# Kernel tuning notes

Measured on AMD Instinct MI355X. Metric: run time of the kernel, lower is better.

## Reference

```python
import jax, jax.numpy as jnp
import numpy as np

N, E = 50000, 400000
FN, FE = 128, 128          # in/out node and edge feature dims
W = 256                     # fnns_width
EPS = 1e-5


def _layer_norm(x, g, b):
    m = x.mean(-1, keepdims=True)
    var = x.var(-1, keepdims=True)
    return (x - m) / jnp.sqrt(var + EPS) * g + b


def _fnn(x, params):
    # FNN applies ReLU after EVERY linear, including the last one.
    for w, b in params:
        x = jax.nn.relu(x @ w + b)
    return x


def setup_inputs() -> dict:
    key = jax.random.key(0)
    ks = jax.random.split(key, 32)
    s = 0.05
    d = {
        'v': jax.random.normal(ks[0], (N, FN), jnp.float32),
        'e': jax.random.normal(ks[1], (E, FE), jnp.float32),
        'edge_index': jax.random.randint(ks[2], (2, E), 0, N, jnp.int32),
        # edge branch: LayerNorm over concat width FE + 2*FN = 384
        'edge_ln_g': jnp.ones((FE + 2 * FN,), jnp.float32),
        'edge_ln_b': jnp.zeros((FE + 2 * FN,), jnp.float32),
        'ew0': jax.random.normal(ks[3], (FE + 2 * FN, W), jnp.float32) * s,
        'eb0': jnp.zeros((W,), jnp.float32),
        'ew1': jax.random.normal(ks[4], (W, W), jnp.float32) * s,
        'eb1': jnp.zeros((W,), jnp.float32),
        'ew2': jax.random.normal(ks[5], (W, FE), jnp.float32) * s,
        'eb2': jnp.zeros((FE,), jnp.float32),
        'edge_linear': jax.random.normal(ks[6], (FE, FE), jnp.float32) * s,
        # node branch: LayerNorm over concat width FE + FN = 256
        'node_ln_g': jnp.ones((FE + FN,), jnp.float32),
        'node_ln_b': jnp.zeros((FE + FN,), jnp.float32),
        'nw0': jax.random.normal(ks[7], (FE + FN, W), jnp.float32) * s,
        'nb0': jnp.zeros((W,), jnp.float32),
        'nw1': jax.random.normal(ks[8], (W, W), jnp.float32) * s,
        'nb1': jnp.zeros((W,), jnp.float32),
        'nw2': jax.random.normal(ks[9], (W, FN), jnp.float32) * s,
        'nb2': jnp.zeros((FN,), jnp.float32),
        'node_linear': jax.random.normal(ks[10], (FN, FN), jnp.float32) * s,
    }
    return d


def reference(v, e, edge_index, edge_ln_g, edge_ln_b, ew0, eb0, ew1, eb1,
              ew2, eb2, edge_linear, node_ln_g, node_ln_b, nw0, nb0, nw1,
              nb1, nw2, nb2, node_linear):
    row, col = edge_index[0], edge_index[1]
    n = v.shape[0]
    # edge update: residual linear + FNN(LayerNorm(concat))
    edge_in = jnp.concatenate([e, v[row], v[col]], axis=-1)  # [E, 384]
    e_new = e @ edge_linear + _fnn(
        _layer_norm(edge_in, edge_ln_g, edge_ln_b),
        [(ew0, eb0), (ew1, eb1), (ew2, eb2)])
    # mean scatter-aggregate over destination nodes (col)
    counts = jax.ops.segment_sum(jnp.ones((e.shape[0],), e.dtype), col,
                                 num_segments=n)
    e_aggr = jax.ops.segment_sum(e_new, col, num_segments=n)
    e_aggr = e_aggr / jnp.clip(counts, 1.0)[:, None]
    # node update
    node_in = jnp.concatenate([e_aggr, v], axis=-1)  # [N, 256]
    v_new = v @ node_linear + _fnn(
        _layer_norm(node_in, node_ln_g, node_ln_b),
        [(nw0, nb0), (nw1, nb1), (nw2, nb2)])
    return (v_new, e_new)
```

## Files before the change

kernel.cpp:

```cpp
#include <hip/hip_runtime.h>

typedef _Float16 f16_t;
typedef f16_t f16x4 __attribute__((ext_vector_type(4)));
typedef f16_t f16x8 __attribute__((ext_vector_type(8)));
typedef float f32x4 __attribute__((ext_vector_type(4)));

#define MFMA16(a, b, c) __builtin_amdgcn_mfma_f32_16x16x32_f16((a), (b), (c), 0, 0, 0)

__device__ __forceinline__ float bfr(float x) { return (float)(__bf16)x; }

__global__ void pack_weights_kernel(
    const float* __restrict__ ew0, const float* __restrict__ ew1,
    const float* __restrict__ ew2, const float* __restrict__ eL,
    const float* __restrict__ nw0, const float* __restrict__ nw1,
    const float* __restrict__ nw2, const float* __restrict__ nL,
    f16_t* __restrict__ dst)
{
    int tid = blockIdx.x * 256 + threadIdx.x;
    int fid = tid >> 6, lane = tid & 63;
    const float* src; int Ncols, foff, doff;
    if (fid < 192)      { src = ew0; Ncols = 256; foff = 0;   doff = 0;      }
    else if (fid < 320) { src = ew1; Ncols = 256; foff = 192; doff = 98304;  }
    else if (fid < 384) { src = ew2; Ncols = 128; foff = 320; doff = 163840; }
    else if (fid < 416) { src = eL;  Ncols = 128; foff = 384; doff = 196608; }
    else if (fid < 544) { src = nw0; Ncols = 256; foff = 416; doff = 212992; }
    else if (fid < 672) { src = nw1; Ncols = 256; foff = 544; doff = 278528; }
    else if (fid < 736) { src = nw2; Ncols = 128; foff = 672; doff = 344064; }
    else                { src = nL;  Ncols = 128; foff = 736; doff = 376832; }
    int f = fid - foff;
    int NT = Ncols >> 4;
    int kstep = f / NT, ntile = f - kstep * NT;
    int col = ntile * 16 + (lane & 15);
    int kbase = kstep * 32 + ((lane >> 4) << 3);
    f16x8 out;
    #pragma unroll
    for (int j = 0; j < 8; ++j)
        out[j] = (f16_t)bfr(src[(size_t)(kbase + j) * Ncols + col]);
    *reinterpret_cast<f16x8*>(dst + (size_t)doff + ((size_t)f * 64 + lane) * 8) = out;
}

__global__ void pack_params_kernel(
    const float* __restrict__ elng, const float* __restrict__ elnb,
    const float* __restrict__ eb0,  const float* __restrict__ eb1,
    const float* __restrict__ eb2,  const float* __restrict__ nlng,
    const float* __restrict__ nlnb, const float* __restrict__ nb0,
    const float* __restrict__ nb1,  const float* __restrict__ nb2,
    float* __restrict__ pp)
{
    int tid = blockIdx.x * 256 + threadIdx.x;
    if (tid >= 2560) return;
    const float* src; int off;
    if (tid < 384)       { src = elng; off = 0; }
    else if (tid < 768)  { src = elnb; off = 384; }
    else if (tid < 1024) { src = eb0;  off = 768; }
    else if (tid < 1280) { src = eb1;  off = 1024; }
    else if (tid < 1408) { src = eb2;  off = 1280; }
    else if (tid < 1664) { src = nlng; off = 1408; }
    else if (tid < 1920) { src = nlnb; off = 1664; }
    else if (tid < 2176) { src = nb0;  off = 1920; }
    else if (tid < 2432) { src = nb1;  off = 2176; }
    else                 { src = nb2;  off = 2432; }
    pp[tid] = bfr(src[tid - off]);
}

__launch_bounds__(1024, 8)
__global__ void edge_kernel(
    const float* __restrict__ vfeat, const float* __restrict__ efeat,
    const int* __restrict__ eidx,
    const float* __restrict__ pp,
    const f16_t* __restrict__ pw,
    float* __restrict__ out_e, float* __restrict__ aggr, float* __restrict__ cnts,
    int Ee)
{
    __shared__ f16_t XF[12 * 4 * 512];
    __shared__ f16_t ERF[4 * 4 * 512];
    __shared__ float SB[64 * 8];
    __shared__ int cidx[64];

    const int t    = threadIdx.x;
    const int lane = t & 63;
    const int wv   = t >> 6;
    const int r16  = lane & 15;
    const int g4i  = lane >> 4;
    const size_t ebase = (size_t)blockIdx.x * 64;

    const int et_  = wv >> 2;
    const int sq4  = wv & 3;
    const int edge = et_ * 16 + r16;
    const int slot = sq4 * 4 + g4i;
    const size_t eg0 = ebase + edge;
    const int r0 = eidx[eg0];
    const int c0 = eidx[(size_t)Ee + eg0];

    f16x8 oct[3];
    float s = 0.f, sq = 0.f;
    {
        const float4* e4 = (const float4*)efeat;
        const float4* v4 = (const float4*)vfeat;
        const float4* srcs[3];
        srcs[0] = &e4[eg0 * 32 + slot * 2];
        srcs[1] = &v4[(size_t)r0 * 32 + slot * 2];
        srcs[2] = &v4[(size_t)c0 * 32 + slot * 2];
        #pragma unroll
        for (int i = 0; i < 3; ++i) {
            float4 f0 = srcs[i][0];
            float4 f1 = srcs[i][1];
            float x0 = bfr(f0.x), x1 = bfr(f0.y), x2 = bfr(f0.z), x3 = bfr(f0.w);
            float x4 = bfr(f1.x), x5 = bfr(f1.y), x6 = bfr(f1.z), x7 = bfr(f1.w);
            s  += x0 + x1 + x2 + x3 + x4 + x5 + x6 + x7;
            sq += x0*x0 + x1*x1 + x2*x2 + x3*x3 + x4*x4 + x5*x5 + x6*x6 + x7*x7;
            f16x8 h;
            h[0] = (f16_t)x0; h[1] = (f16_t)x1; h[2] = (f16_t)x2; h[3] = (f16_t)x3;
            h[4] = (f16_t)x4; h[5] = (f16_t)x5; h[6] = (f16_t)x6; h[7] = (f16_t)x7;
            oct[i] = h;
        }
        *reinterpret_cast<f16x8*>(&ERF[(sq4 * 4 + et_) * 512 + lane * 8]) = oct[0];
        if (slot == 0) {
            cidx[edge] = c0;
            unsafeAtomicAdd(&cnts[c0], 1.0f);
        }
    }
    s  += __shfl_xor(s, 16);  s  += __shfl_xor(s, 32);
    sq += __shfl_xor(sq, 16); sq += __shfl_xor(sq, 32);
    if (g4i == 0)
        *reinterpret_cast<float2*>(&SB[edge * 8 + sq4 * 2]) = make_float2(s, sq);
    __syncthreads();

    {
        float4 p0 = *reinterpret_cast<const float4*>(&SB[edge * 8]);
        float4 p1 = *reinterpret_cast<const float4*>(&SB[edge * 8 + 4]);
        float S = p0.x + p0.z + p1.x + p1.z;
        float Q = p0.y + p0.w + p1.y + p1.w;
        const float mean = S * (1.f / 384.f);
        const float rstd = 1.f / sqrtf(Q * (1.f / 384.f) - mean * mean + 1e-5f);
        const float4* g4p = (const float4*)pp;
        const float4* bpp = (const float4*)(pp + 384);
        #pragma unroll
        for (int i = 0; i < 3; ++i) {
            int q = (i * 16 + slot) * 2;
            float4 g0 = g4p[q], g1 = g4p[q + 1];
            float4 bb0 = bpp[q], bb1 = bpp[q + 1];
            f16x8 h = oct[i];
            f16x8 y;
            float tt, cc;
            tt = rstd * g0.x; cc = bb0.x - mean * tt; y[0] = (f16_t)((float)h[0] * tt + cc);
            tt = rstd * g0.y; cc = bb0.y - mean * tt; y[1] = (f16_t)((float)h[1] * tt + cc);
            tt = rstd * g0.z; cc = bb0.z - mean * tt; y[2] = (f16_t)((float)h[2] * tt + cc);
            tt = rstd * g0.w; cc = bb0.w - mean * tt; y[3] = (f16_t)((float)h[3] * tt + cc);
            tt = rstd * g1.x; cc = bb1.x - mean * tt; y[4] = (f16_t)((float)h[4] * tt + cc);
            tt = rstd * g1.y; cc = bb1.y - mean * tt; y[5] = (f16_t)((float)h[5] * tt + cc);
            tt = rstd * g1.z; cc = bb1.z - mean * tt; y[6] = (f16_t)((float)h[6] * tt + cc);
            tt = rstd * g1.w; cc = bb1.w - mean * tt; y[7] = (f16_t)((float)h[7] * tt + cc);
            int ks = i * 4 + sq4;
            *reinterpret_cast<f16x8*>(&XF[(ks * 4 + et_) * 512 + lane * 8]) = y;
        }
    }
    __syncthreads();

    {
        f32x4 acc[4] = {};
        const f16_t* bw = pw;
        f16x8 wA = *reinterpret_cast<const f16x8*>(&bw[((size_t)(wv) * 64 + lane) * 8]);
        f16x8 wB = *reinterpret_cast<const f16x8*>(&bw[((size_t)(16 + wv) * 64 + lane) * 8]);
        #pragma unroll
        for (int ks = 0; ks < 12; ++ks) {
            f16x8 wN = wB;
            if (ks + 2 < 12)
                wN = *reinterpret_cast<const f16x8*>(
                    &bw[((size_t)((ks + 2) * 16 + wv) * 64 + lane) * 8]);
            #pragma unroll
            for (int et = 0; et < 4; ++et) {
                f16x8 xb = *reinterpret_cast<const f16x8*>(
                    &XF[(ks * 4 + et) * 512 + lane * 8]);
                acc[et] = MFMA16(wA, xb, acc[et]);
            }
            wA = wB; wB = wN;
        }
        __syncthreads();
        float4 bs = *reinterpret_cast<const float4*>(&pp[768 + wv * 16 + g4i * 4]);
        int ks2 = wv >> 1;
        int lane2 = r16 + 16 * ((wv & 1) * 2 + (g4i >> 1));
        int j0 = (g4i & 1) * 4;
        #pragma unroll
        for (int et = 0; et < 4; ++et) {
            f16x4 hv;
            hv[0] = (f16_t)fmaxf(acc[et][0] + bs.x, 0.f);
            hv[1] = (f16_t)fmaxf(acc[et][1] + bs.y, 0.f);
            hv[2] = (f16_t)fmaxf(acc[et][2] + bs.z, 0.f);
            hv[3] = (f16_t)fmaxf(acc[et][3] + bs.w, 0.f);
            *reinterpret_cast<f16x4*>(&XF[(ks2 * 4 + et) * 512 + lane2 * 8 + j0]) = hv;
        }
    }
    __syncthreads();

    {
        f32x4 acc[4] = {};
        const f16_t* bw = pw + 98304;
        f16x8 wA = *reinterpret_cast<const f16x8*>(&bw[((size_t)(wv) * 64 + lane) * 8]);
        f16x8 wB = *reinterpret_cast<const f16x8*>(&bw[((size_t)(16 + wv) * 64 + lane) * 8]);
        #pragma unroll
        for (int ks = 0; ks < 8; ++ks) {
            f16x8 wN = wB;
            if (ks + 2 < 8)
                wN = *reinterpret_cast<const f16x8*>(
                    &bw[((size_t)((ks + 2) * 16 + wv) * 64 + lane) * 8]);
            #pragma unroll
            for (int et = 0; et < 4; ++et) {
                f16x8 xb = *reinterpret_cast<const f16x8*>(
                    &XF[(ks * 4 + et) * 512 + lane * 8]);
                acc[et] = MFMA16(wA, xb, acc[et]);
            }
            wA = wB; wB = wN;
        }
        __syncthreads();
        float4 bs = *reinterpret_cast<const float4*>(&pp[1024 + wv * 16 + g4i * 4]);
        int ks2 = wv >> 1;
        int lane2 = r16 + 16 * ((wv & 1) * 2 + (g4i >> 1));
        int j0 = (g4i & 1) * 4;
        #pragma unroll
        for (int et = 0; et < 4; ++et) {
            f16x4 hv;
            hv[0] = (f16_t)fmaxf(acc[et][0] + bs.x, 0.f);
            hv[1] = (f16_t)fmaxf(acc[et][1] + bs.y, 0.f);
            hv[2] = (f16_t)fmaxf(acc[et][2] + bs.z, 0.f);
            hv[3] = (f16_t)fmaxf(acc[et][3] + bs.w, 0.f);
            *reinterpret_cast<f16x4*>(&XF[(ks2 * 4 + et) * 512 + lane2 * 8 + j0]) = hv;
        }
    }
    __syncthreads();

    {
        const int cw = wv & 7;
        const int rw = wv >> 3;
        f32x4 accF[2] = {}, accR[2] = {};
        const f16_t* bw = pw + 163840;
        f16x8 wA = *reinterpret_cast<const f16x8*>(&bw[((size_t)(cw) * 64 + lane) * 8]);
        f16x8 wB = *reinterpret_cast<const f16x8*>(&bw[((size_t)(8 + cw) * 64 + lane) * 8]);
        #pragma unroll
        for (int ks = 0; ks < 8; ++ks) {
            f16x8 wN = wB;
            if (ks + 2 < 8)
                wN = *reinterpret_cast<const f16x8*>(
                    &bw[((size_t)((ks + 2) * 8 + cw) * 64 + lane) * 8]);
            #pragma unroll
            for (int e2 = 0; e2 < 2; ++e2) {
                f16x8 xa = *reinterpret_cast<const f16x8*>(
                    &XF[(ks * 4 + rw * 2 + e2) * 512 + lane * 8]);
                accF[e2] = MFMA16(xa, wA, accF[e2]);
            }
            wA = wB; wB = wN;
        }
        const f16_t* bwL = pw + 196608;
        f16x8 lA = *reinterpret_cast<const f16x8*>(&bwL[((size_t)(cw) * 64 + lane) * 8]);
        f16x8 lB = *reinterpret_cast<const f16x8*>(&bwL[((size_t)(8 + cw) * 64 + lane) * 8]);
        #pragma unroll
        for (int ks = 0; ks < 4; ++ks) {
            f16x8 lN = lB;
            if (ks + 2 < 4)
                lN = *reinterpret_cast<const f16x8*>(
                    &bwL[((size_t)((ks + 2) * 8 + cw) * 64 + lane) * 8]);
            #pragma unroll
            for (int e2 = 0; e2 < 2; ++e2) {
                f16x8 ea = *reinterpret_cast<const f16x8*>(
                    &ERF[(ks * 4 + rw * 2 + e2) * 512 + lane * 8]);
                accR[e2] = MFMA16(ea, lA, accR[e2]);
            }
            lA = lB; lB = lN;
        }
        int c = cw * 16 + r16;
        float bias = pp[1280 + c];
        #pragma unroll
        for (int e2 = 0; e2 < 2; ++e2)
            #pragma unroll
            for (int qi = 0; qi < 4; ++qi) {
                int rr = (rw * 2 + e2) * 16 + g4i * 4 + qi;
                float val = accR[e2][qi] + fmaxf(accF[e2][qi] + bias, 0.f);
                size_t eg2 = ebase + rr;
                __builtin_nontemporal_store(val, &out_e[eg2 * 128 + c]);
                unsafeAtomicAdd(&aggr[(size_t)cidx[rr] * 128 + c], val);
            }
    }
}

__launch_bounds__(512, 6)
__global__ void node_kernel(
    const float* __restrict__ vfeat, const float* __restrict__ aggr,
    const float* __restrict__ cnts,
    const float* __restrict__ pp,
    const f16_t* __restrict__ pw,
    float* __restrict__ out_v, int Nn)
{
    __shared__ f16_t X[32 * 264];
    __shared__ f16_t H1[32 * 264];

    const int t    = threadIdx.x;
    const int lane = t & 63;
    const int wv   = t >> 6;
    const size_t nbase = (size_t)blockIdx.x * 32;

    const int nl = t >> 4;
    const int pp16 = t & 15;
    const size_t ng = nbase + nl;
    const bool valid = ng < (size_t)Nn;

    float4 d[4];
    float s = 0.f, sq = 0.f;
    {
        float cmax = 1.f;
        if (valid) cmax = fmaxf(cnts[ng], 1.f);
        const float4* a4 = (const float4*)aggr;
        const float4* v4 = (const float4*)vfeat;
        #pragma unroll
        for (int i = 0; i < 4; ++i) {
            int q = i * 16 + pp16;
            float4 r = make_float4(0.f, 0.f, 0.f, 0.f);
            if (valid) {
                if (q < 32) {
                    r = a4[ng * 32 + q];
                    r.x = r.x / cmax; r.y = r.y / cmax;
                    r.z = r.z / cmax; r.w = r.w / cmax;
                } else {
                    float4 rv = v4[ng * 32 + (q - 32)];
                    r.x = bfr(rv.x); r.y = bfr(rv.y); r.z = bfr(rv.z); r.w = bfr(rv.w);
                }
            }
            d[i] = r;
            s  += r.x + r.y + r.z + r.w;
            sq += r.x*r.x + r.y*r.y + r.z*r.z + r.w*r.w;
        }
    }
    #pragma unroll
    for (int off = 1; off < 16; off <<= 1) {
        s  += __shfl_xor(s, off);
        sq += __shfl_xor(sq, off);
    }
    const float mean = s * (1.f / 256.f);
    const float rstd = 1.f / sqrtf(sq * (1.f / 256.f) - mean * mean + 1e-5f);
    {
        const float4* g4p = (const float4*)(pp + 1408);
        const float4* bpp = (const float4*)(pp + 1664);
        #pragma unroll
        for (int i = 0; i < 4; ++i) {
            int q = i * 16 + pp16;
            float4 g = g4p[q]; float4 bb = bpp[q];
            f16x4 y;
            float tt;
            tt = rstd * g.x; y[0] = (f16_t)(d[i].x * tt + (bb.x - mean * tt));
            tt = rstd * g.y; y[1] = (f16_t)(d[i].y * tt + (bb.y - mean * tt));
            tt = rstd * g.z; y[2] = (f16_t)(d[i].z * tt + (bb.z - mean * tt));
            tt = rstd * g.w; y[3] = (f16_t)(d[i].w * tt + (bb.w - mean * tt));
            *reinterpret_cast<f16x4*>(&X[nl * 264 + q * 4]) = y;
        }
    }
    __syncthreads();

    const int r16 = lane & 15;
    const int g4i = lane >> 4;
    const int cb4 = g4i * 4;

    {
        f32x4 acc[2][2] = {};
        const f16_t* bw = pw;
        #pragma unroll
        for (int ks = 0; ks < 8; ++ks) {
            f16x8 wa0 = *reinterpret_cast<const f16x8*>(
                &bw[((size_t)(ks * 16 + wv * 2 + 0) * 64 + lane) * 8]);
            f16x8 wa1 = *reinterpret_cast<const f16x8*>(
                &bw[((size_t)(ks * 16 + wv * 2 + 1) * 64 + lane) * 8]);
            #pragma unroll
            for (int nt = 0; nt < 2; ++nt) {
                f16x8 xb = *reinterpret_cast<const f16x8*>(
                    &X[(nt * 16 + r16) * 264 + ks * 32 + g4i * 8]);
                acc[nt][0] = MFMA16(wa0, xb, acc[nt][0]);
                acc[nt][1] = MFMA16(wa1, xb, acc[nt][1]);
            }
        }
        #pragma unroll
        for (int j = 0; j < 2; ++j) {
            int cb = (wv * 2 + j) * 16 + cb4;
            float4 bs = *reinterpret_cast<const float4*>(&pp[1920 + cb]);
            #pragma unroll
            for (int nt = 0; nt < 2; ++nt) {
                f16x4 hv;
                hv[0] = (f16_t)fmaxf(acc[nt][j][0] + bs.x, 0.f);
                hv[1] = (f16_t)fmaxf(acc[nt][j][1] + bs.y, 0.f);
                hv[2] = (f16_t)fmaxf(acc[nt][j][2] + bs.z, 0.f);
                hv[3] = (f16_t)fmaxf(acc[nt][j][3] + bs.w, 0.f);
                *reinterpret_cast<f16x4*>(&H1[(nt * 16 + r16) * 264 + cb]) = hv;
            }
        }
    }
    __syncthreads();

    {
        f32x4 acc[2][2] = {};
        const f16_t* bw = pw + 65536;
        #pragma unroll
        for (int ks = 0; ks < 8; ++ks) {
            f16x8 wa0 = *reinterpret_cast<const f16x8*>(
                &bw[((size_t)(ks * 16 + wv * 2 + 0) * 64 + lane) * 8]);
            f16x8 wa1 = *reinterpret_cast<const f16x8*>(
                &bw[((size_t)(ks * 16 + wv * 2 + 1) * 64 + lane) * 8]);
            #pragma unroll
            for (int nt = 0; nt < 2; ++nt) {
                f16x8 xb = *reinterpret_cast<const f16x8*>(
                    &H1[(nt * 16 + r16) * 264 + ks * 32 + g4i * 8]);
                acc[nt][0] = MFMA16(wa0, xb, acc[nt][0]);
                acc[nt][1] = MFMA16(wa1, xb, acc[nt][1]);
            }
        }
        __syncthreads();
        #pragma unroll
        for (int j = 0; j < 2; ++j) {
            int cb = (wv * 2 + j) * 16 + cb4;
            float4 bs = *reinterpret_cast<const float4*>(&pp[2176 + cb]);
            #pragma unroll
            for (int nt = 0; nt < 2; ++nt) {
                f16x4 hv;
                hv[0] = (f16_t)fmaxf(acc[nt][j][0] + bs.x, 0.f);
                hv[1] = (f16_t)fmaxf(acc[nt][j][1] + bs.y, 0.f);
                hv[2] = (f16_t)fmaxf(acc[nt][j][2] + bs.z, 0.f);
                hv[3] = (f16_t)fmaxf(acc[nt][j][3] + bs.w, 0.f);
                *reinterpret_cast<f16x4*>(&X[(nt * 16 + r16) * 264 + cb]) = hv;
            }
        }
    }
    __syncthreads();

    {
        f32x4 accF[2] = {}, accR[2] = {};
        const f16_t* bw = pw + 131072;
        #pragma unroll
        for (int ks = 0; ks < 8; ++ks) {
            f16x8 wb = *reinterpret_cast<const f16x8*>(
                &bw[((size_t)(ks * 8 + wv) * 64 + lane) * 8]);
            #pragma unroll
            for (int nt = 0; nt < 2; ++nt) {
                f16x8 xa = *reinterpret_cast<const f16x8*>(
                    &X[(nt * 16 + r16) * 264 + ks * 32 + g4i * 8]);
                accF[nt] = MFMA16(xa, wb, accF[nt]);
            }
        }
        const f16_t* bwL = pw + 163840;
        #pragma unroll
        for (int ks = 0; ks < 4; ++ks) {
            f16x8 wb = *reinterpret_cast<const f16x8*>(
                &bwL[((size_t)(ks * 8 + wv) * 64 + lane) * 8]);
            #pragma unroll
            for (int nt = 0; nt < 2; ++nt) {
                size_t rv = nbase + (size_t)(nt * 16 + r16);
                if (rv >= (size_t)Nn) rv = (size_t)Nn - 1;
                const float4* src = (const float4*)&vfeat[rv * 128 + ks * 32 + g4i * 8];
                float4 f0 = src[0];
                float4 f1 = src[1];
                f16x8 va;
                va[0] = (f16_t)bfr(f0.x); va[1] = (f16_t)bfr(f0.y);
                va[2] = (f16_t)bfr(f0.z); va[3] = (f16_t)bfr(f0.w);
                va[4] = (f16_t)bfr(f1.x); va[5] = (f16_t)bfr(f1.y);
                va[6] = (f16_t)bfr(f1.z); va[7] = (f16_t)bfr(f1.w);
                accR[nt] = MFMA16(va, wb, accR[nt]);
            }
        }
        int c = wv * 16 + r16;
        float bias = pp[2432 + c];
        #pragma unroll
        for (int nt = 0; nt < 2; ++nt)
            #pragma unroll
            for (int qi = 0; qi < 4; ++qi) {
                int rr = nt * 16 + cb4 + qi;
                size_t ng2 = nbase + rr;
                if (ng2 < (size_t)Nn) {
                    float val = accR[nt][qi] + fmaxf(accF[nt][qi] + bias, 0.f);
                    __builtin_nontemporal_store(val, &out_v[ng2 * 128 + c]);
                }
            }
    }
}

extern "C" void kernel_launch(void* const* d_in, const int* in_sizes, int n_in,
                              void* d_out, int out_size, void* d_ws, size_t ws_size,
                              hipStream_t stream)
{
    const float* v    = (const float*)d_in[0];
    const float* e    = (const float*)d_in[1];
    const int*   eidx = (const int*)d_in[2];
    const float* elng = (const float*)d_in[3];
    const float* elnb = (const float*)d_in[4];
    const float* ew0  = (const float*)d_in[5];
    const float* eb0  = (const float*)d_in[6];
    const float* ew1  = (const float*)d_in[7];
    const float* eb1  = (const float*)d_in[8];
    const float* ew2  = (const float*)d_in[9];
    const float* eb2  = (const float*)d_in[10];
    const float* eLin = (const float*)d_in[11];
    const float* nlng = (const float*)d_in[12];
    const float* nlnb = (const float*)d_in[13];
    const float* nw0  = (const float*)d_in[14];
    const float* nb0  = (const float*)d_in[15];
    const float* nw1  = (const float*)d_in[16];
    const float* nb1  = (const float*)d_in[17];
    const float* nw2  = (const float*)d_in[18];
    const float* nb2  = (const float*)d_in[19];
    const float* nLin = (const float*)d_in[20];

    const int Nn = in_sizes[0] / 128;
    const int Ee = in_sizes[1] / 128;

    float* out_v = (float*)d_out;
    float* out_e = out_v + (size_t)Nn * 128;

    float* aggr = (float*)d_ws;
    float* cnts = aggr + (size_t)Nn * 128;
    f16_t* packw = (f16_t*)((char*)d_ws + (size_t)Nn * 129 * 4);
    float* pp = (float*)((char*)packw + 393216 * 2);

    hipMemsetAsync(d_ws, 0, (size_t)Nn * 129 * 4, stream);

    pack_weights_kernel<<<192, 256, 0, stream>>>(ew0, ew1, ew2, eLin,
                                                 nw0, nw1, nw2, nLin, packw);
    pack_params_kernel<<<10, 256, 0, stream>>>(elng, elnb, eb0, eb1, eb2,
                                               nlng, nlnb, nb0, nb1, nb2, pp);

    edge_kernel<<<(Ee + 63) / 64, 1024, 0, stream>>>(v, e, eidx, pp, packw,
                                                     out_e, aggr, cnts, Ee);

    node_kernel<<<(Nn + 31) / 32, 512, 0, stream>>>(v, aggr, cnts, pp,
                                                    packw + 212992, out_v, Nn);
}
```

Baseline: 410.2 us.

## Stage edge outputs in LDS and scatter-add in packed fp16 atomics

Edge outputs are first written to shared memory, then each thread emits vectorized 128-bit stores for out_e. It also performs packed half2 atomic adds into an fp16 aggregation buffer, replacing per-element fp32 atomics. This halves the aggregation buffer, its memset, and the atomic instruction count, and the node kernel reads fp16 sums. The risk is reduced accumulation precision, since fp16 sums of many edge values can lose accuracy or overflow. Two added block barriers also reuse the XF shared buffer.

```diff
diff --git a/kernel.cpp b/kernel.cpp
--- a/kernel.cpp
+++ b/kernel.cpp
@@ -1,4 +1,5 @@
 #include <hip/hip_runtime.h>
+#include <hip/hip_fp16.h>
 
 typedef _Float16 f16_t;
 typedef f16_t f16x4 __attribute__((ext_vector_type(4)));
@@ -69,8 +70,8 @@
     const int* __restrict__ eidx,
     const float* __restrict__ pp,
     const f16_t* __restrict__ pw,
-    float* __restrict__ out_e, float* __restrict__ aggr, float* __restrict__ cnts,
-    int Ee)
+    float* __restrict__ out_e, __half2* __restrict__ aggr16,
+    float* __restrict__ cnts, int Ee)
 {
     __shared__ f16_t XF[12 * 4 * 512];
     __shared__ f16_t ERF[4 * 4 * 512];
@@ -269,22 +270,38 @@
         }
         int c = cw * 16 + r16;
         float bias = pp[1280 + c];
+        float* AG = (float*)XF;
+        __syncthreads();
         #pragma unroll
         for (int e2 = 0; e2 < 2; ++e2)
             #pragma unroll
             for (int qi = 0; qi < 4; ++qi) {
                 int rr = (rw * 2 + e2) * 16 + g4i * 4 + qi;
-                float val = accR[e2][qi] + fmaxf(accF[e2][qi] + bias, 0.f);
-                size_t eg2 = ebase + rr;
-                __builtin_nontemporal_store(val, &out_e[eg2 * 128 + c]);
-                unsafeAtomicAdd(&aggr[(size_t)cidx[rr] * 128 + c], val);
-            }
+                AG[rr * 132 + c] = accR[e2][qi] + fmaxf(accF[e2][qi] + bias, 0.f);
+            }
+    }
+    __syncthreads();
+
+    {
+        const int e2g = t >> 4;
+        const int oc  = t & 15;
+        const float* AG = (const float*)XF;
+        f32x4 a0 = *reinterpret_cast<const f32x4*>(&AG[e2g * 132 + oc * 8]);
+        f32x4 a1 = *reinterpret_cast<const f32x4*>(&AG[e2g * 132 + oc * 8 + 4]);
+        f32x4* op = reinterpret_cast<f32x4*>(&out_e[(ebase + e2g) * 128 + oc * 8]);
+        __builtin_nontemporal_store(a0, op);
+        __builtin_nontemporal_store(a1, op + 1);
+        __half2* ap = &aggr16[(size_t)cidx[e2g] * 64 + oc * 4];
+        unsafeAtomicAdd(ap + 0, __halves2half2(__float2half(a0[0]), __float2half(a0[1])));
+        unsafeAtomicAdd(ap + 1, __halves2half2(__float2half(a0[2]), __float2half(a0[3])));
+        unsafeAtomicAdd(ap + 2, __halves2half2(__float2half(a1[0]), __float2half(a1[1])));
+        unsafeAtomicAdd(ap + 3, __halves2half2(__float2half(a1[2]), __float2half(a1[3])));
     }
 }
 
 __launch_bounds__(512, 6)
 __global__ void node_kernel(
-    const float* __restrict__ vfeat, const float* __restrict__ aggr,
+    const float* __restrict__ vfeat, const f16_t* __restrict__ aggr16f,
     const float* __restrict__ cnts,
     const float* __restrict__ pp,
     const f16_t* __restrict__ pw,
@@ -308,7 +325,7 @@
     {
         float cmax = 1.f;
         if (valid) cmax = fmaxf(cnts[ng], 1.f);
-        const float4* a4 = (const float4*)aggr;
+        float inv = 1.f / cmax;
         const float4* v4 = (const float4*)vfeat;
         #pragma unroll
         for (int i = 0; i < 4; ++i) {
@@ -316,9 +333,9 @@
             float4 r = make_float4(0.f, 0.f, 0.f, 0.f);
             if (valid) {
                 if (q < 32) {
-                    r = a4[ng * 32 + q];
-                    r.x = r.x / cmax; r.y = r.y / cmax;
-                    r.z = r.z / cmax; r.w = r.w / cmax;
+                    f16x4 hv = *reinterpret_cast<const f16x4*>(&aggr16f[ng * 128 + q * 4]);
+                    r.x = (float)hv[0] * inv; r.y = (float)hv[1] * inv;
+                    r.z = (float)hv[2] * inv; r.w = (float)hv[3] * inv;
                 } else {
                     float4 rv = v4[ng * 32 + (q - 32)];
                     r.x = bfr(rv.x); r.y = bfr(rv.y); r.z = bfr(rv.z); r.w = bfr(rv.w);
@@ -509,12 +526,13 @@
     float* out_v = (float*)d_out;
     float* out_e = out_v + (size_t)Nn * 128;
 
-    float* aggr = (float*)d_ws;
-    float* cnts = aggr + (size_t)Nn * 128;
-    f16_t* packw = (f16_t*)((char*)d_ws + (size_t)Nn * 129 * 4);
-    float* pp = (float*)((char*)packw + 393216 * 2);
-
-    hipMemsetAsync(d_ws, 0, (size_t)Nn * 129 * 4, stream);
+    __half2* aggr16 = (__half2*)d_ws;
+    f16_t*   aggr16f = (f16_t*)d_ws;
+    float*   cnts = (float*)((char*)d_ws + (size_t)Nn * 128 * 2);
+    f16_t*   packw = (f16_t*)((char*)d_ws + (size_t)Nn * 128 * 2 + (size_t)Nn * 4);
+    float*   pp = (float*)((char*)packw + 393216 * 2);
+
+    hipMemsetAsync(d_ws, 0, (size_t)Nn * 128 * 2 + (size_t)Nn * 4, stream);
 
     pack_weights_kernel<<<192, 256, 0, stream>>>(ew0, ew1, ew2, eLin,
                                                  nw0, nw1, nw2, nLin, packw);
@@ -522,8 +540,8 @@
                                                nlng, nlnb, nb0, nb1, nb2, pp);
 
     edge_kernel<<<(Ee + 63) / 64, 1024, 0, stream>>>(v, e, eidx, pp, packw,
-                                                     out_e, aggr, cnts, Ee);
-
-    node_kernel<<<(Nn + 31) / 32, 512, 0, stream>>>(v, aggr, cnts, pp,
+                                                     out_e, aggr16, cnts, Ee);
+
+    node_kernel<<<(Nn + 31) / 32, 512, 0, stream>>>(v, aggr16f, cnts, pp,
                                                     packw + 212992, out_v, Nn);
 }
```

Measured after the change: 544.3 us. +32.7%, slower.
